# Kernel tuning notes

Measured on AMD Instinct MI355X. Metric: run time of the kernel, lower is better.

## Reference

```python
import jax, jax.numpy as jnp
import numpy as np

B, F_IN, HID, H, S = 256, 1024, 1024, 16, 128
TEMP = float((HID // H) ** 0.5)  # 8.0


def setup_inputs() -> dict:
    key = jax.random.key(0)
    ks = jax.random.split(key, 7)
    return {
        "x": jax.random.normal(ks[0], (B, F_IN, S), dtype=jnp.float32),
        "Wq": jax.random.normal(ks[1], (HID, F_IN), dtype=jnp.float32) * (1.0 / np.sqrt(F_IN)),
        "bq": jax.random.normal(ks[2], (HID,), dtype=jnp.float32) * 0.01,
        "Wk": jax.random.normal(ks[3], (HID, F_IN), dtype=jnp.float32) * (1.0 / np.sqrt(F_IN)),
        "bk": jax.random.normal(ks[4], (HID,), dtype=jnp.float32) * 0.01,
        "Wo": jax.random.normal(ks[5], (S,), dtype=jnp.float32) * (1.0 / np.sqrt(S)),
        "bo": jax.random.normal(ks[6], (1,), dtype=jnp.float32) * 0.01,
    }


def _to_heads(t):
    # (B, F, S) -> (B, H, S, F//H), matching reshape(B,H,F/H,S).permute(0,1,3,2)
    b, f, s = t.shape
    return t.reshape(b, H, f // H, s).transpose(0, 1, 3, 2)


def reference(x, Wq, bq, Wk, bk, Wo, bo):
    # 1x1 Conv1d == per-position linear over channel dim
    q = jnp.einsum('bis,hi->bhs', x, Wq) + bq[None, :, None]
    k = jnp.einsum('bis,hi->bhs', x, Wk) + bk[None, :, None]
    qh = _to_heads(q)          # (B,H,S,HID/H)
    kh = _to_heads(k)          # (B,H,S,HID/H)
    vh = _to_heads(x)          # (B,H,S,F_IN/H)  -- v is the raw input, unprojected
    scores = jnp.einsum('bhsd,bhtd->bhst', qh, kh) / TEMP
    attn = jax.nn.softmax(scores, axis=-1)
    out = jnp.einsum('bhst,bhtd->bhsd', attn, vh)   # (B,H,S,F_IN/H)
    # _reshape_from_batches: (B,H,S,dv) -> (B, F_IN, S)
    out = out.transpose(0, 1, 3, 2).reshape(x.shape[0], F_IN, S)
    # map_o: Linear(num_users, 1) over last axis, then squeeze
    score = jnp.einsum('bfs,s->bf', out, Wo) + bo[0]
    return score
```

## Files before the change

### kernel.cpp

```cpp
#include <hip/hip_runtime.h>

#define F 1024
#define S 128
#define H 16
#define D 64
#define CK 64
#define NCHUNK 16

typedef short bf16x8 __attribute__((ext_vector_type(8)));
typedef float f32x4  __attribute__((ext_vector_type(4)));

#define XS_UNITS ((size_t)128 * NCHUNK * 2048)
#define WB_UNITS ((size_t)8 * NCHUNK * 2048)
#define WS_NEED ((XS_UNITS + WB_UNITS) * 16)

#define MAIN_LDS_BYTES (8192 * 16 + 8 * 128 * 4 + 128 * 4)

__device__ __forceinline__ unsigned short f2bf(float f) {
    unsigned u = __float_as_uint(f);
    u += 0x7fffu + ((u >> 16) & 1u);
    return (unsigned short)(u >> 16);
}

__device__ __forceinline__ uint4 pack8(const float* f) {
    uint4 u;
    u.x = (unsigned)f2bf(f[0]) | ((unsigned)f2bf(f[1]) << 16);
    u.y = (unsigned)f2bf(f[2]) | ((unsigned)f2bf(f[3]) << 16);
    u.z = (unsigned)f2bf(f[4]) | ((unsigned)f2bf(f[5]) << 16);
    u.w = (unsigned)f2bf(f[6]) | ((unsigned)f2bf(f[7]) << 16);
    return u;
}

typedef __attribute__((address_space(1))) const unsigned int as1_u32;
typedef __attribute__((address_space(3))) unsigned int as3_u32;

__device__ __forceinline__ void async_cp16(const uint4* g, uint4* l) {
    __builtin_amdgcn_global_load_lds((as1_u32*)g, (as3_u32*)l, 16, 0, 0);
}

__device__ __forceinline__ void bar()   { __builtin_amdgcn_s_barrier(); }
__device__ __forceinline__ void sb0()   { __builtin_amdgcn_sched_barrier(0); }
__device__ __forceinline__ void lgkm0() { asm volatile("s_waitcnt lgkmcnt(0)"); }

template<int N> __device__ __forceinline__ void vmw() {
    asm volatile("s_waitcnt vmcnt(%0)" :: "n"(N));
}

__global__ void prep(const float* __restrict__ x,
                     const float* __restrict__ Wq,
                     const float* __restrict__ Wk,
                     uint4* __restrict__ xs,
                     uint4* __restrict__ wb)
{
    __shared__ float4 t4[64 * 33];
    const int tid = threadIdx.x;
    const int blk = blockIdx.x;
    if (blk < 4096) {
        const int b = blk >> 4, ch = blk & 15;
        const float4* src = (const float4*)(x + ((size_t)b * F + ch * CK) * S);
        float4 v[8];
#pragma unroll
        for (int j = 0; j < 8; ++j) v[j] = src[tid + j * 256];
#pragma unroll
        for (int j = 0; j < 8; ++j) {
            const int e4 = tid + j * 256;
            t4[(e4 >> 5) * 33 + (e4 & 31)] = v[j];
        }
        __syncthreads();
        const float* tile = (const float*)t4;
        uint4* dst = xs + ((size_t)(b >> 1) * NCHUNK + ch) * 2048 + (b & 1) * 128;
#pragma unroll
        for (int j = 0; j < 4; ++j) {
            const int u  = tid + j * 256;
            const int kc = u >> 7;
            const int s  = u & 127;
            float f[8];
#pragma unroll
            for (int jj = 0; jj < 8; ++jj) f[jj] = tile[(kc * 8 + jj) * 132 + s];
            dst[kc * 256 + s] = pack8(f);
        }
    } else {
        const int blk2 = blk - 4096;
        const int h = blk2 >> 4, ch = blk2 & 15;
        uint4* dst = wb + ((size_t)(h >> 1) * NCHUNK + ch) * 2048 + (h & 1) * 128;
#pragma unroll
        for (int j = 0; j < 4; ++j) {
            const int u  = tid + j * 256;
            const int kc = u >> 7;
            const int m  = u & 127;
            const float* srcp = (m < 64)
                ? (Wq + (size_t)(h * D + m) * F + ch * CK + kc * 8)
                : (Wk + (size_t)(h * D + m - 64) * F + ch * CK + kc * 8);
            float f[8];
            float4 a = ((const float4*)srcp)[0];
            float4 c = ((const float4*)srcp)[1];
            f[0] = a.x; f[1] = a.y; f[2] = a.z; f[3] = a.w;
            f[4] = c.x; f[5] = c.y; f[6] = c.z; f[7] = c.w;
            dst[kc * 256 + m] = pack8(f);
        }
    }
}

__device__ __forceinline__ void read4(const uint4* mat, int base, bf16x8 (&r)[4]) {
    r[0] = *(const bf16x8*)&mat[base];
    r[1] = *(const bf16x8*)&mat[base + 16];
    r[2] = *(const bf16x8*)&mat[base + 32];
    r[3] = *(const bf16x8*)&mat[base + 48];
}

template<int RB>
__device__ __forceinline__ void mfma16(f32x4 (&acc)[8][4], const bf16x8 (&af)[4], const bf16x8 (&br)[4]) {
#pragma unroll
    for (int mt = 0; mt < 4; ++mt)
#pragma unroll
        for (int nt = 0; nt < 4; ++nt)
            acc[RB + mt][nt] = __builtin_amdgcn_mfma_f32_16x16x32_bf16(af[mt], br[nt], acc[RB + mt][nt], 0, 0, 0);
}

template<int HALF>
__device__ __forceinline__ void stage_half(uint4* mat, const uint4* wbase, const uint4* xbase,
                                           int tgt, int wv, int lane) {
    const int bufb = (tgt & 1) * 4096;
    const uint4* g;
    int l;
    if constexpr (HALF == 0)      { g = wbase + (size_t)tgt * 2048;        l = bufb;        }
    else if constexpr (HALF == 1) { g = xbase + (size_t)tgt * 2048;        l = bufb + 2048; }
    else if constexpr (HALF == 2) { g = wbase + (size_t)tgt * 2048 + 1024; l = bufb + 1024; }
    else                          { g = xbase + (size_t)tgt * 2048 + 1024; l = bufb + 3072; }
    async_cp16(g + wv * 128 + lane,      &mat[l + wv * 128]);
    async_cp16(g + wv * 128 + 64 + lane, &mat[l + wv * 128 + 64]);
}

template<int CUR, bool I1, bool I2, int W1, int W2, bool DW2>
__device__ __forceinline__ void ktile(uint4* mat, const uint4* wbase, const uint4* xbase,
                                      int t, int wv, int lane, int wm, int wn, int q, int l15,
                                      f32x4 (&acc)[8][4])
{
    bf16x8 af[4], br[4];
    const int abase = CUR * 4096 + wm * 128 + l15;
    const int bbase = CUR * 4096 + 2048 + wn * 64 + l15;
    const int kq = q * 256;
    read4(mat, abase + kq, af);
    read4(mat, bbase + kq, br);
    if constexpr (I1) stage_half<2>(mat, wbase, xbase, t + 1, wv, lane);
    bar(); lgkm0(); sb0();
    __builtin_amdgcn_s_setprio(1); mfma16<0>(acc, af, br); __builtin_amdgcn_s_setprio(0);
    bar(); sb0();
    read4(mat, abase + kq + 64, af);
    if constexpr (I1) stage_half<3>(mat, wbase, xbase, t + 1, wv, lane);
    bar(); lgkm0(); sb0();
    __builtin_amdgcn_s_setprio(1); mfma16<4>(acc, af, br); __builtin_amdgcn_s_setprio(0);
    vmw<W1>(); bar(); sb0();
    read4(mat, abase + kq + 1024, af);
    read4(mat, bbase + kq + 1024, br);
    if constexpr (I2) stage_half<0>(mat, wbase, xbase, t + 2, wv, lane);
    bar(); lgkm0(); sb0();
    __builtin_amdgcn_s_setprio(1); mfma16<0>(acc, af, br); __builtin_amdgcn_s_setprio(0);
    bar(); sb0();
    read4(mat, abase + kq + 1024 + 64, af);
    if constexpr (I2) stage_half<1>(mat, wbase, xbase, t + 2, wv, lane);
    bar(); lgkm0(); sb0();
    __builtin_amdgcn_s_setprio(1); mfma16<4>(acc, af, br); __builtin_amdgcn_s_setprio(0);
    if constexpr (DW2) { vmw<W2>(); bar(); sb0(); }
}

__launch_bounds__(512, 2)
__global__ void attn_main(const float* __restrict__ x,
                          const uint4* __restrict__ xs,
                          const uint4* __restrict__ wb,
                          const float* __restrict__ bq,
                          const float* __restrict__ bk,
                          const float* __restrict__ Wo,
                          const float* __restrict__ bo,
                          float* __restrict__ out)
{
    (void)x;
    extern __shared__ char smraw[];
    uint4* mat   = (uint4*)smraw;
    float* wpart = (float*)(smraw + 8192 * 16);

    const int tid  = threadIdx.x;
    const int lane = tid & 63;
    const int wv   = tid >> 6;
    const int l15  = lane & 15;
    const int q    = lane >> 4;
    const int wm   = wv >> 2;
    const int wn   = wv & 3;

    const int g    = blockIdx.x;
    const int xcd  = g & 7;
    const int slot = g >> 3;
    const int bg   = xcd * 16 + (slot & 15);
    const int hg   = slot >> 4;

    const uint4* wbase = wb + (size_t)hg * NCHUNK * 2048;
    const uint4* xbase = xs + (size_t)bg * NCHUNK * 2048;

    f32x4 acc[8][4];
#pragma unroll
    for (int mi = 0; mi < 8; ++mi)
#pragma unroll
        for (int ni = 0; ni < 4; ++ni) acc[mi][ni] = (f32x4){0.f, 0.f, 0.f, 0.f};

    stage_half<0>(mat, wbase, xbase, 0, wv, lane);
    stage_half<1>(mat, wbase, xbase, 0, wv, lane);
    stage_half<2>(mat, wbase, xbase, 0, wv, lane);
    stage_half<3>(mat, wbase, xbase, 0, wv, lane);
    stage_half<0>(mat, wbase, xbase, 1, wv, lane);
    stage_half<1>(mat, wbase, xbase, 1, wv, lane);
    vmw<8>();
    bar(); sb0();

#pragma unroll 1
    for (int i = 0; i < 7; ++i) {
        ktile<0, true, true, 8, 8, true>(mat, wbase, xbase, 2 * i,     wv, lane, wm, wn, q, l15, acc);
        ktile<1, true, true, 8, 8, true>(mat, wbase, xbase, 2 * i + 1, wv, lane, wm, wn, q, l15, acc);
    }
    ktile<0, true,  false, 8, 4, true >(mat, wbase, xbase, 14, wv, lane, wm, wn, q, l15, acc);
    ktile<1, false, false, 0, 0, false>(mat, wbase, xbase, 15, wv, lane, wm, wn, q, l15, acc);

    __syncthreads();

    {
        unsigned short* m16 = (unsigned short*)mat;
        const int hglobw = hg * 2 + wm;
#pragma unroll
        for (int rt = 0; rt < 8; ++rt) {
            const int mh0   = rt * 16 + q * 4;
            const int d0    = mh0 & 63;
            const int kbase = (mh0 < 64) ? 0 : 1024;
            float bias4[4];
#pragma unroll
            for (int rr = 0; rr < 4; ++rr)
                bias4[rr] = (mh0 < 64) ? bq[hglobw * D + d0 + rr] : bk[hglobw * D + d0 + rr];
#pragma unroll
            for (int ct = 0; ct < 4; ++ct) {
                const int col = wn * 64 + ct * 16 + l15;
                const int bj  = col >> 7;
                const int s   = col & 127;
                const int c   = wm * 2 + bj;
                unsigned long long pv = 0;
#pragma unroll
                for (int rr = 0; rr < 4; ++rr)
                    pv |= (unsigned long long)f2bf(acc[rt][ct][rr] + bias4[rr]) << (16 * rr);
                const int unit = c * 2048 + kbase + s * 8 + ((d0 >> 3) ^ (s & 7));
                *(unsigned long long*)&m16[unit * 8 + (d0 & 7)] = pv;
            }
        }
    }
    __syncthreads();

    const int ce   = ((wv >> 2) << 1) | ((wv >> 1) & 1);
    const int half = wv & 1;
    const int qb = ce * 2048;
    const int kb = ce * 2048 + 1024;
    const int bglob = bg * 2 + (ce & 1);
    const int hglob = hg * 2 + (ce >> 1);

    f32x4 p[4][8];
#pragma unroll
    for (int mt = 0; mt < 4; ++mt)
#pragma unroll
        for (int nt = 0; nt < 8; ++nt) p[mt][nt] = (f32x4){0.f, 0.f, 0.f, 0.f};
#pragma unroll
    for (int ks = 0; ks < 2; ++ks) {
        const int kcq = ks * 4 + q;
        bf16x8 a2[4], b2[8];
#pragma unroll
        for (int mt = 0; mt < 4; ++mt) {
            const int row = half * 64 + mt * 16 + l15;
            a2[mt] = *(const bf16x8*)&mat[qb + row * 8 + (kcq ^ (row & 7))];
        }
#pragma unroll
        for (int nt = 0; nt < 8; ++nt) {
            const int trow = nt * 16 + l15;
            b2[nt] = *(const bf16x8*)&mat[kb + trow * 8 + (kcq ^ (trow & 7))];
        }
#pragma unroll
        for (int mt = 0; mt < 4; ++mt)
#pragma unroll
            for (int nt = 0; nt < 8; ++nt)
                p[mt][nt] = __builtin_amdgcn_mfma_f32_16x16x32_bf16(a2[mt], b2[nt], p[mt][nt], 0, 0, 0);
    }

    const int ell = half * 64 + lane;
    const int kc5 = ell >> 4;
    const int sg5 = ell & 15;
    const uint4* xsrc = xbase + (size_t)hglob * 2048 + kc5 * 256 + (ce & 1) * 128 + sg5 * 8;
    uint4 xu[8];
#pragma unroll
    for (int jj = 0; jj < 8; ++jj) xu[jj] = xsrc[jj];

    float pw[8];
#pragma unroll
    for (int nt = 0; nt < 8; ++nt) pw[nt] = 0.f;
#pragma unroll
    for (int mt = 0; mt < 4; ++mt) {
#pragma unroll
        for (int rr = 0; rr < 4; ++rr) {
            const int srow = half * 64 + mt * 16 + q * 4 + rr;
            float e[8];
            float l = 0.f;
#pragma unroll
            for (int nt = 0; nt < 8; ++nt) {
                e[nt] = __expf(fminf(p[mt][nt][rr] * 0.125f, 80.f));
                l += e[nt];
            }
#pragma unroll
            for (int off = 1; off < 16; off <<= 1) l += __shfl_xor(l, off);
            const float cw = Wo[srow] / l;
#pragma unroll
            for (int nt = 0; nt < 8; ++nt) pw[nt] = fmaf(cw, e[nt], pw[nt]);
        }
    }
#pragma unroll
    for (int nt = 0; nt < 8; ++nt) {
        pw[nt] += __shfl_xor(pw[nt], 16);
        pw[nt] += __shfl_xor(pw[nt], 32);
    }
    if (q == 0) {
#pragma unroll
        for (int nt = 0; nt < 8; ++nt) wpart[wv * 128 + nt * 16 + l15] = pw[nt];
    }
    __syncthreads();

    {
        const float* w0 = wpart + 2 * ce * 128;
        const float* w1 = w0 + 128;
        float acc8[8];
#pragma unroll
        for (int e = 0; e < 8; ++e) acc8[e] = 0.f;
#pragma unroll
        for (int jj = 0; jj < 8; ++jj) {
            const int s = sg5 * 8 + jj;
            const float w = w0[s] + w1[s];
            const unsigned* du = (const unsigned*)&xu[jj];
#pragma unroll
            for (int dw = 0; dw < 4; ++dw) {
                const unsigned v = du[dw];
                acc8[dw * 2 + 0] = fmaf(__uint_as_float(v << 16), w, acc8[dw * 2 + 0]);
                acc8[dw * 2 + 1] = fmaf(__uint_as_float(v & 0xffff0000u), w, acc8[dw * 2 + 1]);
            }
        }
#pragma unroll
        for (int e = 0; e < 8; ++e) {
#pragma unroll
            for (int off = 1; off < 16; off <<= 1)
                acc8[e] += __shfl_xor(acc8[e], off);
        }
        if (sg5 < 8)
            out[(size_t)bglob * F + hglob * D + kc5 * 8 + sg5] = acc8[sg5] + bo[0];
    }
}

struct SmemT {
    uint4 mat[2048];
    float wpart[4][S];
    float wfin[S];
};

__launch_bounds__(256, 4)
__global__ void attn_fallback(const float* __restrict__ x,
                              const float* __restrict__ Wq,
                              const float* __restrict__ bq,
                              const float* __restrict__ Wk,
                              const float* __restrict__ bk,
                              const float* __restrict__ Wo,
                              const float* __restrict__ bo,
                              float* __restrict__ out)
{
    __shared__ SmemT sm;
    const int tid  = threadIdx.x;
    const int lane = tid & 63;
    const int wv   = tid >> 6;
    const int l15  = lane & 15;
    const int q    = lane >> 4;

    const int g    = blockIdx.x;
    const int xcd  = g & 7;
    const int slot = g >> 3;
    const int hg   = slot >> 7;
    const int r0   = slot & 127;
    const int b    = xcd * 32 + (r0 >> 2);
    const int h    = hg * 4 + (r0 & 3);

    const float* xb  = x  + (size_t)b * (F * S);
    const float* wqh = Wq + (size_t)h * D * F;
    const float* wkh = Wk + (size_t)h * D * F;

    const int m0 = (wv & 1) * 64;
    const int n0 = (wv >> 1) * 64;

    f32x4 acc[4][4];
#pragma unroll
    for (int mt = 0; mt < 4; ++mt)
#pragma unroll
        for (int nt = 0; nt < 4; ++nt) acc[mt][nt] = (f32x4){0.f, 0.f, 0.f, 0.f};

    const int mq  = tid >> 2;
    const int kq  = tid & 3;
    const int s0x = (tid & 63) * 2;
    const int iq  = tid >> 6;

    for (int ch = 0; ch < NCHUNK; ++ch) {
        const int c0 = ch * CK;
        __syncthreads();
        {
            const int key = mq & 7;
            float f[16];
            const float4* srcq = (const float4*)(wqh + (size_t)mq * F + (c0 + kq * 16));
#pragma unroll
            for (int j = 0; j < 4; ++j) {
                float4 v = srcq[j];
                f[4*j] = v.x; f[4*j+1] = v.y; f[4*j+2] = v.z; f[4*j+3] = v.w;
            }
            sm.mat[mq * 8 + ((kq * 2    ) ^ key)] = pack8(f);
            sm.mat[mq * 8 + ((kq * 2 + 1) ^ key)] = pack8(f + 8);
            const float4* srck = (const float4*)(wkh + (size_t)mq * F + (c0 + kq * 16));
#pragma unroll
            for (int j = 0; j < 4; ++j) {
                float4 v = srck[j];
                f[4*j] = v.x; f[4*j+1] = v.y; f[4*j+2] = v.z; f[4*j+3] = v.w;
            }
            sm.mat[(64 + mq) * 8 + ((kq * 2    ) ^ key)] = pack8(f);
            sm.mat[(64 + mq) * 8 + ((kq * 2 + 1) ^ key)] = pack8(f + 8);
        }
        {
            const float* src = xb + (size_t)(c0 + iq * 16) * S + s0x;
            float fa[8], fb[8];
#pragma unroll
            for (int grp = 0; grp < 2; ++grp) {
#pragma unroll
                for (int j = 0; j < 8; ++j) {
                    float2 v = *(const float2*)(src + (size_t)(grp * 8 + j) * S);
                    fa[j] = v.x; fb[j] = v.y;
                }
                const int kc = iq * 2 + grp;
                sm.mat[1024 + (s0x    ) * 8 + (kc ^ ((s0x    ) & 7))] = pack8(fa);
                sm.mat[1024 + (s0x + 1) * 8 + (kc ^ ((s0x + 1) & 7))] = pack8(fb);
            }
        }
        __syncthreads();
#pragma unroll
        for (int ks = 0; ks < 2; ++ks) {
            bf16x8 af[4], br[4];
#pragma unroll
            for (int mt = 0; mt < 4; ++mt) {
                const int row = m0 + mt * 16 + l15;
                af[mt] = *(const bf16x8*)&sm.mat[row * 8 + ((ks * 4 + q) ^ (row & 7))];
            }
#pragma unroll
            for (int nt = 0; nt < 4; ++nt) {
                const int row = n0 + nt * 16 + l15;
                br[nt] = *(const bf16x8*)&sm.mat[1024 + row * 8 + ((ks * 4 + q) ^ (row & 7))];
            }
#pragma unroll
            for (int mt = 0; mt < 4; ++mt)
#pragma unroll
                for (int nt = 0; nt < 4; ++nt)
                    acc[mt][nt] = __builtin_amdgcn_mfma_f32_16x16x32_bf16(
                        af[mt], br[nt], acc[mt][nt], 0, 0, 0);
        }
    }

    __syncthreads();
    {
        unsigned short* m16 = (unsigned short*)sm.mat;
#pragma unroll
        for (int mt = 0; mt < 4; ++mt) {
#pragma unroll
            for (int rr = 0; rr < 4; ++rr) {
                const int m = m0 + mt * 16 + q * 4 + rr;
                const int d = m & 63;
                const float bias = (m < 64) ? bq[h * D + d] : bk[h * D + d];
                const int base = (m < 64) ? 0 : 8192;
#pragma unroll
                for (int nt = 0; nt < 4; ++nt) {
                    const int s = n0 + nt * 16 + l15;
                    const float v = acc[mt][nt][rr] + bias;
                    const int unit = s * 8 + (((d >> 3)) ^ (s & 7));
                    m16[base + unit * 8 + (d & 7)] = f2bf(v);
                }
            }
        }
    }
    __syncthreads();

    f32x4 p[2][8];
#pragma unroll
    for (int mt = 0; mt < 2; ++mt)
#pragma unroll
        for (int nt = 0; nt < 8; ++nt) p[mt][nt] = (f32x4){0.f, 0.f, 0.f, 0.f};

#pragma unroll
    for (int ks = 0; ks < 2; ++ks) {
        bf16x8 a2[2], b2[8];
#pragma unroll
        for (int mt = 0; mt < 2; ++mt) {
            const int row = wv * 32 + mt * 16 + l15;
            a2[mt] = *(const bf16x8*)&sm.mat[row * 8 + ((ks * 4 + q) ^ (row & 7))];
        }
#pragma unroll
        for (int nt = 0; nt < 8; ++nt) {
            const int row = nt * 16 + l15;
            b2[nt] = *(const bf16x8*)&sm.mat[1024 + row * 8 + ((ks * 4 + q) ^ (row & 7))];
        }
#pragma unroll
        for (int mt = 0; mt < 2; ++mt)
#pragma unroll
            for (int nt = 0; nt < 8; ++nt)
                p[mt][nt] = __builtin_amdgcn_mfma_f32_16x16x32_bf16(a2[mt], b2[nt], p[mt][nt], 0, 0, 0);
    }

    float pw[8];
#pragma unroll
    for (int nt = 0; nt < 8; ++nt) pw[nt] = 0.f;

#pragma unroll
    for (int mt = 0; mt < 2; ++mt) {
#pragma unroll
        for (int rr = 0; rr < 4; ++rr) {
            const int srow = wv * 32 + mt * 16 + q * 4 + rr;
            float mx = p[mt][0][rr];
#pragma unroll
            for (int nt = 1; nt < 8; ++nt) mx = fmaxf(mx, p[mt][nt][rr]);
#pragma unroll
            for (int off = 1; off < 16; off <<= 1) mx = fmaxf(mx, __shfl_xor(mx, off));
            float e[8];
            float l = 0.f;
#pragma unroll
            for (int nt = 0; nt < 8; ++nt) {
                e[nt] = __expf((p[mt][nt][rr] - mx) * 0.125f);
                l += e[nt];
            }
#pragma unroll
            for (int off = 1; off < 16; off <<= 1) l += __shfl_xor(l, off);
            const float c = Wo[srow] / l;
#pragma unroll
            for (int nt = 0; nt < 8; ++nt) pw[nt] = fmaf(c, e[nt], pw[nt]);
        }
    }
#pragma unroll
    for (int nt = 0; nt < 8; ++nt) {
        pw[nt] += __shfl_xor(pw[nt], 16);
        pw[nt] += __shfl_xor(pw[nt], 32);
    }
    if (q == 0) {
#pragma unroll
        for (int nt = 0; nt < 8; ++nt) sm.wpart[wv][nt * 16 + l15] = pw[nt];
    }
    __syncthreads();
    if (tid < S)
        sm.wfin[tid] = sm.wpart[0][tid] + sm.wpart[1][tid] + sm.wpart[2][tid] + sm.wpart[3][tid];
    __syncthreads();

    {
        const int dd   = tid >> 2;
        const int part = tid & 3;
        const float* xv = xb + (size_t)(h * D + dd) * S + part * 32;
        float a5 = 0.f;
#pragma unroll 8
        for (int t = 0; t < 32; ++t) a5 = fmaf(sm.wfin[part * 32 + t], xv[t], a5);
        a5 += __shfl_xor(a5, 1);
        a5 += __shfl_xor(a5, 2);
        if (part == 0) out[(size_t)b * F + h * D + dd] = a5 + bo[0];
    }
}

extern "C" void kernel_launch(void* const* d_in, const int* in_sizes, int n_in,
                              void* d_out, int out_size, void* d_ws, size_t ws_size,
                              hipStream_t stream) {
    const float* x  = (const float*)d_in[0];
    const float* Wq = (const float*)d_in[1];
    const float* bq = (const float*)d_in[2];
    const float* Wk = (const float*)d_in[3];
    const float* bk = (const float*)d_in[4];
    const float* Wo = (const float*)d_in[5];
    const float* bo = (const float*)d_in[6];
    float* out = (float*)d_out;

    if (ws_size >= WS_NEED) {
        uint4* xsp = (uint4*)d_ws;
        uint4* wbp = (uint4*)((char*)d_ws + XS_UNITS * 16);
        static bool attr_done = false;
        if (!attr_done) {
            (void)hipFuncSetAttribute(reinterpret_cast<const void*>(attn_main),
                                      hipFuncAttributeMaxDynamicSharedMemorySize, MAIN_LDS_BYTES);
            attr_done = true;
        }
        prep<<<dim3(4096 + 256), dim3(256), 0, stream>>>(x, Wq, Wk, xsp, wbp);
        attn_main<<<dim3(1024), dim3(512), MAIN_LDS_BYTES, stream>>>(x, xsp, wbp, bq, bk, Wo, bo, out);
    } else {
        attn_fallback<<<dim3(256 * H), dim3(256), 0, stream>>>(x, Wq, bq, Wk, bk, Wo, bo, out);
    }
}
```

Baseline: 353.0 us.

## Restructure GEMM k-tile pipeline with fewer barriers and partial LDS waits

The main GEMM loop is rewritten so each half-tile reads all A/B fragments up front and uses partial lgkmcnt waits instead of full waits plus barriers between every MFMA group. This cuts per-tile barriers from eight to two and lets the first MFMA group start while later LDS reads are still in flight. It also tightens the vmcnt waits for the new staging order. Separately, the prep kernel drops its LDS transpose and reads x with strided global loads directly. Fewer barriers raise the risk of LDS buffer races, and the uncoalesced prep reads may cost more memory traffic.

```diff
diff --git a/kernel.cpp b/kernel.cpp
--- a/kernel.cpp
+++ b/kernel.cpp
@@ -40,8 +40,10 @@
 
 __device__ __forceinline__ void bar()   { __builtin_amdgcn_s_barrier(); }
 __device__ __forceinline__ void sb0()   { __builtin_amdgcn_sched_barrier(0); }
-__device__ __forceinline__ void lgkm0() { asm volatile("s_waitcnt lgkmcnt(0)"); }
-
+
+template<int N> __device__ __forceinline__ void lgkm() {
+    asm volatile("s_waitcnt lgkmcnt(%0)" :: "n"(N));
+}
 template<int N> __device__ __forceinline__ void vmw() {
     asm volatile("s_waitcnt vmcnt(%0)" :: "n"(N));
 }
@@ -52,31 +54,21 @@
                      uint4* __restrict__ xs,
                      uint4* __restrict__ wb)
 {
-    __shared__ float4 t4[64 * 33];
     const int tid = threadIdx.x;
     const int blk = blockIdx.x;
     if (blk < 4096) {
         const int b = blk >> 4, ch = blk & 15;
-        const float4* src = (const float4*)(x + ((size_t)b * F + ch * CK) * S);
-        float4 v[8];
-#pragma unroll
-        for (int j = 0; j < 8; ++j) v[j] = src[tid + j * 256];
-#pragma unroll
-        for (int j = 0; j < 8; ++j) {
-            const int e4 = tid + j * 256;
-            t4[(e4 >> 5) * 33 + (e4 & 31)] = v[j];
-        }
-        __syncthreads();
-        const float* tile = (const float*)t4;
+        const float* xb = x + ((size_t)b * F + ch * CK) * S;
         uint4* dst = xs + ((size_t)(b >> 1) * NCHUNK + ch) * 2048 + (b & 1) * 128;
 #pragma unroll
         for (int j = 0; j < 4; ++j) {
             const int u  = tid + j * 256;
             const int kc = u >> 7;
             const int s  = u & 127;
+            const float* rp = xb + (size_t)(kc * 8) * S + s;
             float f[8];
 #pragma unroll
-            for (int jj = 0; jj < 8; ++jj) f[jj] = tile[(kc * 8 + jj) * 132 + s];
+            for (int jj = 0; jj < 8; ++jj) f[jj] = rp[jj * S];
             dst[kc * 256 + s] = pack8(f);
         }
     } else {
@@ -131,37 +123,46 @@
     async_cp16(g + wv * 128 + 64 + lane, &mat[l + wv * 128 + 64]);
 }
 
-template<int CUR, bool I1, bool I2, int W1, int W2, bool DW2>
-__device__ __forceinline__ void ktile(uint4* mat, const uint4* wbase, const uint4* xbase,
-                                      int t, int wv, int lane, int wm, int wn, int q, int l15,
-                                      f32x4 (&acc)[8][4])
+template<int CUR, int SMODE>
+__device__ __forceinline__ void ktile2(uint4* mat, const uint4* wbase, const uint4* xbase,
+                                       int t, int wv, int lane, int wm, int wn, int q, int l15,
+                                       f32x4 (&acc)[8][4])
 {
-    bf16x8 af[4], br[4];
-    const int abase = CUR * 4096 + wm * 128 + l15;
-    const int bbase = CUR * 4096 + 2048 + wn * 64 + l15;
-    const int kq = q * 256;
-    read4(mat, abase + kq, af);
-    read4(mat, bbase + kq, br);
-    if constexpr (I1) stage_half<2>(mat, wbase, xbase, t + 1, wv, lane);
-    bar(); lgkm0(); sb0();
-    __builtin_amdgcn_s_setprio(1); mfma16<0>(acc, af, br); __builtin_amdgcn_s_setprio(0);
+    const int ab = CUR * 4096 + wm * 128 + l15 + q * 256;
+    const int bb = CUR * 4096 + 2048 + wn * 64 + l15 + q * 256;
+    {
+        bf16x8 a0[4], a1[4], b0[4];
+        read4(mat, ab, a0);
+        read4(mat, bb, b0);
+        read4(mat, ab + 64, a1);
+        sb0();
+        if constexpr (SMODE >= 1) stage_half<2>(mat, wbase, xbase, t + 1, wv, lane);
+        sb0();
+        lgkm<4>(); sb0();
+        __builtin_amdgcn_s_setprio(1); mfma16<0>(acc, a0, b0); __builtin_amdgcn_s_setprio(0); sb0();
+        if constexpr (SMODE >= 1) stage_half<3>(mat, wbase, xbase, t + 1, wv, lane);
+        sb0();
+        lgkm<0>(); sb0();
+        __builtin_amdgcn_s_setprio(1); mfma16<4>(acc, a1, b0); __builtin_amdgcn_s_setprio(0); sb0();
+    }
+    if constexpr (SMODE >= 1) { vmw<4>(); } else { vmw<0>(); }
     bar(); sb0();
-    read4(mat, abase + kq + 64, af);
-    if constexpr (I1) stage_half<3>(mat, wbase, xbase, t + 1, wv, lane);
-    bar(); lgkm0(); sb0();
-    __builtin_amdgcn_s_setprio(1); mfma16<4>(acc, af, br); __builtin_amdgcn_s_setprio(0);
-    vmw<W1>(); bar(); sb0();
-    read4(mat, abase + kq + 1024, af);
-    read4(mat, bbase + kq + 1024, br);
-    if constexpr (I2) stage_half<0>(mat, wbase, xbase, t + 2, wv, lane);
-    bar(); lgkm0(); sb0();
-    __builtin_amdgcn_s_setprio(1); mfma16<0>(acc, af, br); __builtin_amdgcn_s_setprio(0);
+    {
+        bf16x8 a2[4], a3[4], b1[4];
+        read4(mat, ab + 1024, a2);
+        read4(mat, bb + 1024, b1);
+        read4(mat, ab + 1024 + 64, a3);
+        sb0();
+        if constexpr (SMODE == 2) stage_half<0>(mat, wbase, xbase, t + 2, wv, lane);
+        sb0();
+        lgkm<4>(); sb0();
+        __builtin_amdgcn_s_setprio(1); mfma16<0>(acc, a2, b1); __builtin_amdgcn_s_setprio(0); sb0();
+        if constexpr (SMODE == 2) stage_half<1>(mat, wbase, xbase, t + 2, wv, lane);
+        sb0();
+        lgkm<0>(); sb0();
+        __builtin_amdgcn_s_setprio(1); mfma16<4>(acc, a3, b1); __builtin_amdgcn_s_setprio(0); sb0();
+    }
     bar(); sb0();
-    read4(mat, abase + kq + 1024 + 64, af);
-    if constexpr (I2) stage_half<1>(mat, wbase, xbase, t + 2, wv, lane);
-    bar(); lgkm0(); sb0();
-    __builtin_amdgcn_s_setprio(1); mfma16<4>(acc, af, br); __builtin_amdgcn_s_setprio(0);
-    if constexpr (DW2) { vmw<W2>(); bar(); sb0(); }
 }
 
 __launch_bounds__(512, 2)
@@ -208,16 +209,16 @@
     stage_half<3>(mat, wbase, xbase, 0, wv, lane);
     stage_half<0>(mat, wbase, xbase, 1, wv, lane);
     stage_half<1>(mat, wbase, xbase, 1, wv, lane);
-    vmw<8>();
+    vmw<4>();
     bar(); sb0();
 
 #pragma unroll 1
     for (int i = 0; i < 7; ++i) {
-        ktile<0, true, true, 8, 8, true>(mat, wbase, xbase, 2 * i,     wv, lane, wm, wn, q, l15, acc);
-        ktile<1, true, true, 8, 8, true>(mat, wbase, xbase, 2 * i + 1, wv, lane, wm, wn, q, l15, acc);
-    }
-    ktile<0, true,  false, 8, 4, true >(mat, wbase, xbase, 14, wv, lane, wm, wn, q, l15, acc);
-    ktile<1, false, false, 0, 0, false>(mat, wbase, xbase, 15, wv, lane, wm, wn, q, l15, acc);
+        ktile2<0, 2>(mat, wbase, xbase, 2 * i,     wv, lane, wm, wn, q, l15, acc);
+        ktile2<1, 2>(mat, wbase, xbase, 2 * i + 1, wv, lane, wm, wn, q, l15, acc);
+    }
+    ktile2<0, 1>(mat, wbase, xbase, 14, wv, lane, wm, wn, q, l15, acc);
+    ktile2<1, 0>(mat, wbase, xbase, 15, wv, lane, wm, wn, q, l15, acc);
 
     __syncthreads();
 
```

Measured after the change: 342.1 us. 1.03x faster.
